# Kernel tuning notes

Measured on AMD Instinct MI355X. Metric: run time of the kernel, lower is better.

The kernel has to match this reference:

```python
import jax, jax.numpy as jnp
import numpy as np

N_NODES = 50000
N_EDGES = 640000
IN_F = 128
OUT_F = 32
HEADS = 4
ALPHA = 0.2  # leakyrelu negative slope


def setup_inputs() -> dict:
    key = jax.random.key(0)
    ks = jax.random.split(key, 9)
    xavier = lambda k, shape: jax.random.uniform(
        k, shape, jnp.float32, -1.0, 1.0) * (1.414 * np.sqrt(6.0 / (shape[0] + np.prod(shape[1:]))))
    return {
        "edge_index": jax.random.randint(ks[0], (2, N_EDGES), 0, N_NODES),
        "h": jax.random.normal(ks[1], (N_NODES, IN_F), jnp.float32),
        "edge_feat": jax.random.normal(ks[2], (N_EDGES, IN_F), jnp.float32),
        "W": xavier(ks[3], (IN_F, OUT_F * HEADS)),
        "W_e": xavier(ks[4], (IN_F, OUT_F * HEADS)),
        "a_src": xavier(ks[5], (1, HEADS, OUT_F)),
        "a_dst": xavier(ks[6], (1, HEADS, OUT_F)),
        "a_edge": xavier(ks[7], (1, HEADS, OUT_F)),
    }


def reference(edge_index, h, edge_feat, W, W_e, a_src, a_dst, a_edge):
    N = h.shape[0]
    Wh = (h @ W).reshape(N, HEADS, OUT_F)               # [N,H,D]
    We = (edge_feat @ W_e).reshape(-1, HEADS, OUT_F)    # [E,H,D]
    src, dst = edge_index[0], edge_index[1]
    Wh_src = Wh[src]                                    # [E,H,D] gather
    Wh_dst = Wh[dst]                                    # [E,H,D] gather
    e = ((Wh_src * a_src).sum(-1) + (Wh_dst * a_dst).sum(-1)
         + (We * a_edge).sum(-1))                       # [E,H]
    e = jnp.where(e >= 0, e, ALPHA * e)                 # leaky relu
    attention = jax.nn.softmax(e, axis=0)               # global softmax over edges (as in original)
    msg = attention[:, :, None] * Wh_src                # [E,H,D]
    h_prime = jax.ops.segment_sum(msg, dst, num_segments=N)  # scatter-add per dst
    h_prime = jax.nn.relu(h_prime)
    return h_prime.reshape(N, HEADS * OUT_F)
```

## Files before the change

kernel.cpp:

```cpp
#include <hip/hip_runtime.h>


typedef __attribute__((ext_vector_type(8))) short short8;
typedef __attribute__((ext_vector_type(4))) float f32x4;

#define ALPHA 0.2f
#define CAP 64

__device__ __forceinline__ unsigned short f2bf(float f) {
    unsigned u = __float_as_uint(f);
    u += 0x7fffu + ((u >> 16) & 1u);
    return (unsigned short)(u >> 16);
}
__device__ __forceinline__ float bf2f(unsigned short u) {
    return __uint_as_float(((unsigned)u) << 16);
}

__global__ __launch_bounds__(256) void gemm_wh(const float* __restrict__ hmat,
                                               const float* __restrict__ W,
                                               const float* __restrict__ a_src,
                                               const float* __restrict__ a_dst,
                                               const float* __restrict__ We,
                                               const float* __restrict__ a_edge,
                                               float* __restrict__ Bfold,
                                               int* __restrict__ cnt,
                                               unsigned short* __restrict__ Whb,
                                               float* __restrict__ s_src,
                                               float* __restrict__ s_dst, int N) {
    int tid = threadIdx.x;
    for (int i = blockIdx.x * 256 + tid; i < N; i += (int)gridDim.x * 256)
        cnt[i] = 0;
    if (blockIdx.x == 0 && tid < 128) {
        int k = tid;
        for (int h = 0; h < 4; h++) {
            float acc = 0.f;
            for (int d = 0; d < 32; d++)
                acc += We[k * 128 + h * 32 + d] * a_edge[h * 32 + d];
            Bfold[k * 4 + h] = acc;
        }
    }
    __shared__ short Wb[16384];
    for (int i = tid; i < 16384; i += 256) {
        int j = i & 7, lane = (i >> 3) & 63, ks = (i >> 9) & 3, nt = (i >> 11) & 7;
        int m = lane & 15, quad = lane >> 4;
        int k = ks * 32 + quad * 8 + j;
        int c = nt * 16 + m;
        Wb[i] = (short)f2bf(W[k * 128 + c]);
    }
    __syncthreads();
    int wave = tid >> 6, lane = tid & 63;
    int m = lane & 15, quad = lane >> 4;
    int row0 = blockIdx.x * 64 + wave * 16;
    int row = row0 + m;
    if (row >= N) row = N - 1;
    const float* hrow = hmat + (size_t)row * 128;
    short8 af[4];
    for (int ks = 0; ks < 4; ks++) {
        f32x4 lo = *(const f32x4*)(hrow + ks * 32 + quad * 8);
        f32x4 hi = *(const f32x4*)(hrow + ks * 32 + quad * 8 + 4);
        short8 a;
        a[0] = (short)f2bf(lo.x); a[1] = (short)f2bf(lo.y);
        a[2] = (short)f2bf(lo.z); a[3] = (short)f2bf(lo.w);
        a[4] = (short)f2bf(hi.x); a[5] = (short)f2bf(hi.y);
        a[6] = (short)f2bf(hi.z); a[7] = (short)f2bf(hi.w);
        af[ks] = a;
    }
    float ssrc[4] = {0.f, 0.f, 0.f, 0.f};
    float sdst[4] = {0.f, 0.f, 0.f, 0.f};
    for (int nt = 0; nt < 8; nt++) {
        f32x4 acc = {0.f, 0.f, 0.f, 0.f};
        for (int ks = 0; ks < 4; ks++) {
            short8 bf = *(const short8*)(Wb + ((nt * 4 + ks) * 64 + lane) * 8);
            acc = __builtin_amdgcn_mfma_f32_16x16x32_bf16(af[ks], bf, acc, 0, 0, 0);
        }
        float as = a_src[nt * 16 + m];
        float ad = a_dst[nt * 16 + m];
#pragma unroll
        for (int r = 0; r < 4; r++) {
            int orow = row0 + quad * 4 + r;
            if (orow < N) Whb[(size_t)orow * 128 + nt * 16 + m] = f2bf(acc[r]);
            ssrc[r] += acc[r] * as;
            sdst[r] += acc[r] * ad;
        }
        if (nt & 1) {
#pragma unroll
            for (int off = 1; off < 16; off <<= 1) {
#pragma unroll
                for (int r = 0; r < 4; r++) {
                    ssrc[r] += __shfl_xor(ssrc[r], off);
                    sdst[r] += __shfl_xor(sdst[r], off);
                }
            }
            if (m == 0) {
                int h = nt >> 1;
#pragma unroll
                for (int r = 0; r < 4; r++) {
                    int orow = row0 + quad * 4 + r;
                    if (orow < N) {
                        s_src[(size_t)orow * 4 + h] = ssrc[r];
                        s_dst[(size_t)orow * 4 + h] = sdst[r];
                    }
                }
            }
#pragma unroll
            for (int r = 0; r < 4; r++) { ssrc[r] = 0.f; sdst[r] = 0.f; }
        }
    }
}

__global__ __launch_bounds__(256) void edge_kernel(
        const int* __restrict__ ei, const float* __restrict__ ef,
        const float* __restrict__ Bfold, const float* __restrict__ s_src,
        const float* __restrict__ s_dst, int* __restrict__ cnt,
        int* __restrict__ bsrc, f32x4* __restrict__ bp,
        float* __restrict__ P, int E) {
    __shared__ float psh[16];
    int tid = threadIdx.x;
    long e = (long)blockIdx.x * 256 + tid;
    bool valid = e < E;
    float p0 = 0.f, p1 = 0.f, p2 = 0.f, p3 = 0.f;
    if (valid) {
        float a0 = 0.f, a1 = 0.f, a2 = 0.f, a3 = 0.f;
        const f32x4* xr = (const f32x4*)(ef + (size_t)e * 128);
        const f32x4* B4 = (const f32x4*)Bfold;
#pragma unroll 8
        for (int ch = 0; ch < 32; ch++) {
            f32x4 xv = xr[ch];
#pragma unroll
            for (int j = 0; j < 4; j++) {
                float xf = xv[j];
                f32x4 b = B4[ch * 4 + j];
                a0 += xf * b.x; a1 += xf * b.y; a2 += xf * b.z; a3 += xf * b.w;
            }
        }
        int srcn = ei[e];
        int dstn = ei[(size_t)E + e];
        f32x4 svs = ((const f32x4*)s_src)[srcn];
        f32x4 svd = ((const f32x4*)s_dst)[dstn];
        float t0 = a0 + svs.x + svd.x;
        float t1 = a1 + svs.y + svd.y;
        float t2 = a2 + svs.z + svd.z;
        float t3 = a3 + svs.w + svd.w;
        t0 = t0 >= 0.f ? t0 : ALPHA * t0;
        t1 = t1 >= 0.f ? t1 : ALPHA * t1;
        t2 = t2 >= 0.f ? t2 : ALPHA * t2;
        t3 = t3 >= 0.f ? t3 : ALPHA * t3;
        p0 = expf(t0); p1 = expf(t1); p2 = expf(t2); p3 = expf(t3);
        int pos = atomicAdd(&cnt[dstn], 1);
        if (pos < CAP) {
            size_t slot = (size_t)dstn * CAP + pos;
            bsrc[slot] = srcn;
            f32x4 pv = {p0, p1, p2, p3};
            bp[slot] = pv;
        }
    }
    float r0 = p0, r1 = p1, r2 = p2, r3 = p3;
#pragma unroll
    for (int off = 32; off > 0; off >>= 1) {
        r0 += __shfl_xor(r0, off);
        r1 += __shfl_xor(r1, off);
        r2 += __shfl_xor(r2, off);
        r3 += __shfl_xor(r3, off);
    }
    if ((tid & 63) == 0) {
        int w = tid >> 6;
        psh[w * 4 + 0] = r0; psh[w * 4 + 1] = r1;
        psh[w * 4 + 2] = r2; psh[w * 4 + 3] = r3;
    }
    __syncthreads();
    if (tid < 4)
        P[(size_t)blockIdx.x * 4 + tid] = psh[tid] + psh[4 + tid] + psh[8 + tid] + psh[12 + tid];
}

__global__ void reduce_sums(const float* __restrict__ P, float* __restrict__ sums, int nb) {
    __shared__ float red[256];
    int t = threadIdx.x;
    float acc = 0.f;
    for (int b = t >> 2; b < nb; b += 64) acc += P[(size_t)b * 4 + (t & 3)];
    red[t] = acc;
    __syncthreads();
    for (int s = 128; s >= 4; s >>= 1) {
        if (t < s) red[t] += red[t + s];
        __syncthreads();
    }
    if (t < 4) sums[t] = red[t];
}

__global__ __launch_bounds__(256) void agg_kernel(
        const int* __restrict__ cnt, const int* __restrict__ bsrc,
        const float* __restrict__ bp, const unsigned short* __restrict__ Whb,
        const float* __restrict__ sums, float* __restrict__ out, int N) {
    int wave = threadIdx.x >> 6, lane = threadIdx.x & 63;
    int n = blockIdx.x * 4 + wave;
    if (n >= N) return;
    int m = cnt[n]; if (m > CAP) m = CAP;
    size_t b0 = (size_t)n * CAP;
    int head = lane >> 4;
    float acc0 = 0.f, acc1 = 0.f;
    for (int i = 0; i < m; i += 4) {
        int4 s4 = *(const int4*)(bsrc + b0 + i);
        int rem = m - i;
        int s0 = s4.x;
        int s1 = rem > 1 ? s4.y : s4.x;
        int s2 = rem > 2 ? s4.z : s4.x;
        int s3 = rem > 3 ? s4.w : s4.x;
        float q0 = bp[(b0 + i) * 4 + head];
        float q1 = rem > 1 ? bp[(b0 + i + 1) * 4 + head] : 0.f;
        float q2 = rem > 2 ? bp[(b0 + i + 2) * 4 + head] : 0.f;
        float q3 = rem > 3 ? bp[(b0 + i + 3) * 4 + head] : 0.f;
        unsigned w0 = *(const unsigned*)(Whb + (size_t)s0 * 128 + lane * 2);
        unsigned w1 = *(const unsigned*)(Whb + (size_t)s1 * 128 + lane * 2);
        unsigned w2 = *(const unsigned*)(Whb + (size_t)s2 * 128 + lane * 2);
        unsigned w3 = *(const unsigned*)(Whb + (size_t)s3 * 128 + lane * 2);
        acc0 += q0 * bf2f((unsigned short)(w0 & 0xffffu))
              + q1 * bf2f((unsigned short)(w1 & 0xffffu))
              + q2 * bf2f((unsigned short)(w2 & 0xffffu))
              + q3 * bf2f((unsigned short)(w3 & 0xffffu));
        acc1 += q0 * bf2f((unsigned short)(w0 >> 16))
              + q1 * bf2f((unsigned short)(w1 >> 16))
              + q2 * bf2f((unsigned short)(w2 >> 16))
              + q3 * bf2f((unsigned short)(w3 >> 16));
    }
    float inv = 1.0f / sums[head];
    float2 o;
    o.x = fmaxf(acc0, 0.f) * inv;
    o.y = fmaxf(acc1, 0.f) * inv;
    *(float2*)(out + (size_t)n * 128 + lane * 2) = o;
}

extern "C" void kernel_launch(void* const* d_in, const int* in_sizes, int n_in,
                              void* d_out, int out_size, void* d_ws, size_t ws_size,
                              hipStream_t stream) {
    const int* ei = (const int*)d_in[0];
    const float* hmat = (const float*)d_in[1];
    const float* ef = (const float*)d_in[2];
    const float* W = (const float*)d_in[3];
    const float* We = (const float*)d_in[4];
    const float* a_src = (const float*)d_in[5];
    const float* a_dst = (const float*)d_in[6];
    const float* a_edge = (const float*)d_in[7];
    int E = in_sizes[0] / 2;
    int N = in_sizes[1] / 128;
    int nEdgeBlocks = (E + 255) / 256;

    char* ws = (char*)d_ws;
    size_t off_b = 0;
    auto alloc = [&](size_t bytes) -> void* {
        void* p = ws + off_b;
        off_b = (off_b + bytes + 255) & ~(size_t)255;
        return p;
    };
    unsigned short* Whb = (unsigned short*)alloc((size_t)N * 128 * 2);
    float* s_src = (float*)alloc((size_t)N * 4 * 4);
    float* s_dst = (float*)alloc((size_t)N * 4 * 4);
    float* Bfold = (float*)alloc(128 * 4 * 4);
    int* cnt = (int*)alloc((size_t)N * 4);
    int* bsrc = (int*)alloc((size_t)N * CAP * 4);
    float* bp = (float*)alloc((size_t)N * CAP * 16);
    float* P = (float*)alloc((size_t)nEdgeBlocks * 4 * 4);
    float* sums = (float*)alloc(256);

    gemm_wh<<<(N + 63) / 64, 256, 0, stream>>>(hmat, W, a_src, a_dst, We, a_edge,
                                               Bfold, cnt, Whb, s_src, s_dst, N);
    edge_kernel<<<nEdgeBlocks, 256, 0, stream>>>(ei, ef, Bfold, s_src, s_dst,
                                                 cnt, bsrc, (f32x4*)bp, P, E);
    reduce_sums<<<1, 256, 0, stream>>>(P, sums, nEdgeBlocks);
    agg_kernel<<<(N + 3) / 4, 256, 0, stream>>>(cnt, bsrc, bp, Whb, sums,
                                                (float*)d_out, N);
}
```

Baseline: 570.1 us.

## Run edge-feature dot product concurrently with node GEMM in one fused launch

Moves the edge_feat·(W_e a_edge) reduction out of the edge kernel into extra blocks of the node GEMM launch, so the large edge-feature stream (E×128 floats) is read alongside the node GEMM rather than after it. Each dot block recomputes the folded 128×4 vector into shared memory, and per-edge scores go to a new E×4 buffer that the slimmer edge kernel reads back. The cost is an extra write and read of that score buffer plus redundant folding work in every dot block, in exchange for overlapping the two bandwidth-bound phases.

```diff
diff --git a/kernel.cpp b/kernel.cpp
--- a/kernel.cpp
+++ b/kernel.cpp
@@ -16,29 +16,49 @@
     return __uint_as_float(((unsigned)u) << 16);
 }
 
-__global__ __launch_bounds__(256) void gemm_wh(const float* __restrict__ hmat,
-                                               const float* __restrict__ W,
-                                               const float* __restrict__ a_src,
-                                               const float* __restrict__ a_dst,
-                                               const float* __restrict__ We,
-                                               const float* __restrict__ a_edge,
-                                               float* __restrict__ Bfold,
-                                               int* __restrict__ cnt,
-                                               unsigned short* __restrict__ Whb,
-                                               float* __restrict__ s_src,
-                                               float* __restrict__ s_dst, int N) {
+__global__ __launch_bounds__(256) void fused_gemm_dot(
+        const float* __restrict__ hmat, const float* __restrict__ W,
+        const float* __restrict__ a_src, const float* __restrict__ a_dst,
+        const float* __restrict__ We, const float* __restrict__ a_edge,
+        const float* __restrict__ ef, f32x4* __restrict__ escore,
+        int* __restrict__ cnt, unsigned short* __restrict__ Whb,
+        float* __restrict__ s_src, float* __restrict__ s_dst,
+        int N, int E, int dotBlocks) {
     int tid = threadIdx.x;
     for (int i = blockIdx.x * 256 + tid; i < N; i += (int)gridDim.x * 256)
         cnt[i] = 0;
-    if (blockIdx.x == 0 && tid < 128) {
-        int k = tid;
-        for (int h = 0; h < 4; h++) {
+
+    if ((int)blockIdx.x < dotBlocks) {
+        __shared__ float Bl[512];
+        for (int idx = tid; idx < 512; idx += 256) {
+            int k = idx >> 2, h = idx & 3;
             float acc = 0.f;
             for (int d = 0; d < 32; d++)
                 acc += We[k * 128 + h * 32 + d] * a_edge[h * 32 + d];
-            Bfold[k * 4 + h] = acc;
-        }
-    }
+            Bl[idx] = acc;
+        }
+        __syncthreads();
+        long e = (long)blockIdx.x * 256 + tid;
+        if (e < E) {
+            float a0 = 0.f, a1 = 0.f, a2 = 0.f, a3 = 0.f;
+            const f32x4* xr = (const f32x4*)(ef + (size_t)e * 128);
+            const f32x4* B4 = (const f32x4*)Bl;
+#pragma unroll 8
+            for (int ch = 0; ch < 32; ch++) {
+                f32x4 xv = xr[ch];
+#pragma unroll
+                for (int j = 0; j < 4; j++) {
+                    float xf = xv[j];
+                    f32x4 b = B4[ch * 4 + j];
+                    a0 += xf * b.x; a1 += xf * b.y; a2 += xf * b.z; a3 += xf * b.w;
+                }
+            }
+            f32x4 s = {a0, a1, a2, a3};
+            escore[e] = s;
+        }
+        return;
+    }
+
     __shared__ short Wb[16384];
     for (int i = tid; i < 16384; i += 256) {
         int j = i & 7, lane = (i >> 3) & 63, ks = (i >> 9) & 3, nt = (i >> 11) & 7;
@@ -48,9 +68,10 @@
         Wb[i] = (short)f2bf(W[k * 128 + c]);
     }
     __syncthreads();
+    int gb = (int)blockIdx.x - dotBlocks;
     int wave = tid >> 6, lane = tid & 63;
     int m = lane & 15, quad = lane >> 4;
-    int row0 = blockIdx.x * 64 + wave * 16;
+    int row0 = gb * 64 + wave * 16;
     int row = row0 + m;
     if (row >= N) row = N - 1;
     const float* hrow = hmat + (size_t)row * 128;
@@ -108,11 +129,10 @@
     }
 }
 
-__global__ __launch_bounds__(256) void edge_kernel(
-        const int* __restrict__ ei, const float* __restrict__ ef,
-        const float* __restrict__ Bfold, const float* __restrict__ s_src,
-        const float* __restrict__ s_dst, int* __restrict__ cnt,
-        int* __restrict__ bsrc, f32x4* __restrict__ bp,
+__global__ __launch_bounds__(256) void edge_final(
+        const int* __restrict__ ei, const f32x4* __restrict__ escore,
+        const float* __restrict__ s_src, const float* __restrict__ s_dst,
+        int* __restrict__ cnt, int* __restrict__ bsrc, f32x4* __restrict__ bp,
         float* __restrict__ P, int E) {
     __shared__ float psh[16];
     int tid = threadIdx.x;
@@ -120,27 +140,15 @@
     bool valid = e < E;
     float p0 = 0.f, p1 = 0.f, p2 = 0.f, p3 = 0.f;
     if (valid) {
-        float a0 = 0.f, a1 = 0.f, a2 = 0.f, a3 = 0.f;
-        const f32x4* xr = (const f32x4*)(ef + (size_t)e * 128);
-        const f32x4* B4 = (const f32x4*)Bfold;
-#pragma unroll 8
-        for (int ch = 0; ch < 32; ch++) {
-            f32x4 xv = xr[ch];
-#pragma unroll
-            for (int j = 0; j < 4; j++) {
-                float xf = xv[j];
-                f32x4 b = B4[ch * 4 + j];
-                a0 += xf * b.x; a1 += xf * b.y; a2 += xf * b.z; a3 += xf * b.w;
-            }
-        }
         int srcn = ei[e];
         int dstn = ei[(size_t)E + e];
+        f32x4 a = escore[e];
         f32x4 svs = ((const f32x4*)s_src)[srcn];
         f32x4 svd = ((const f32x4*)s_dst)[dstn];
-        float t0 = a0 + svs.x + svd.x;
-        float t1 = a1 + svs.y + svd.y;
-        float t2 = a2 + svs.z + svd.z;
-        float t3 = a3 + svs.w + svd.w;
+        float t0 = a.x + svs.x + svd.x;
+        float t1 = a.y + svs.y + svd.y;
+        float t2 = a.z + svs.z + svd.z;
+        float t3 = a.w + svs.w + svd.w;
         t0 = t0 >= 0.f ? t0 : ALPHA * t0;
         t1 = t1 >= 0.f ? t1 : ALPHA * t1;
         t2 = t2 >= 0.f ? t2 : ALPHA * t2;
@@ -241,7 +249,8 @@
     const float* a_edge = (const float*)d_in[7];
     int E = in_sizes[0] / 2;
     int N = in_sizes[1] / 128;
-    int nEdgeBlocks = (E + 255) / 256;
+    int dotBlocks = (E + 255) / 256;
+    int gemmBlocks = (N + 63) / 64;
 
     char* ws = (char*)d_ws;
     size_t off_b = 0;
@@ -253,18 +262,19 @@
     unsigned short* Whb = (unsigned short*)alloc((size_t)N * 128 * 2);
     float* s_src = (float*)alloc((size_t)N * 4 * 4);
     float* s_dst = (float*)alloc((size_t)N * 4 * 4);
-    float* Bfold = (float*)alloc(128 * 4 * 4);
+    f32x4* escore = (f32x4*)alloc((size_t)E * 16);
     int* cnt = (int*)alloc((size_t)N * 4);
     int* bsrc = (int*)alloc((size_t)N * CAP * 4);
     float* bp = (float*)alloc((size_t)N * CAP * 16);
-    float* P = (float*)alloc((size_t)nEdgeBlocks * 4 * 4);
+    float* P = (float*)alloc((size_t)dotBlocks * 4 * 4);
     float* sums = (float*)alloc(256);
 
-    gemm_wh<<<(N + 63) / 64, 256, 0, stream>>>(hmat, W, a_src, a_dst, We, a_edge,
-                                               Bfold, cnt, Whb, s_src, s_dst, N);
-    edge_kernel<<<nEdgeBlocks, 256, 0, stream>>>(ei, ef, Bfold, s_src, s_dst,
-                                                 cnt, bsrc, (f32x4*)bp, P, E);
-    reduce_sums<<<1, 256, 0, stream>>>(P, sums, nEdgeBlocks);
+    fused_gemm_dot<<<dotBlocks + gemmBlocks, 256, 0, stream>>>(
+        hmat, W, a_src, a_dst, We, a_edge, ef, escore, cnt, Whb, s_src, s_dst,
+        N, E, dotBlocks);
+    edge_final<<<dotBlocks, 256, 0, stream>>>(ei, escore, s_src, s_dst,
+                                              cnt, bsrc, (f32x4*)bp, P, E);
+    reduce_sums<<<1, 256, 0, stream>>>(P, sums, dotBlocks);
     agg_kernel<<<(N + 3) / 4, 256, 0, stream>>>(cnt, bsrc, bp, Whb, sums,
                                                 (float*)d_out, N);
 }
```

New measurement: 580.4 us. Within noise of the previous version (+1.8%).
